# Performance work log

Hardware: AMD Instinct MI355X
Metric: run time of the kernel (lower is better)

Reference implementation:

```python
import jax, jax.numpy as jnp
import numpy as np


def _sepconv1x1(x, dw, pw, b):
    # SeparableConv2D with kernel=1: depthwise 1x1 = per-channel scale, then pointwise matmul
    return jnp.einsum('nhwc,cd->nhwd', x * dw, pw) + b


def setup_inputs() -> dict:
    key = jax.random.key(0)
    ks = jax.random.split(key, 12)
    N, H, W, C_in, C_red = 4, 64, 64, 256, 64
    s = 0.05  # small init so softmax logits are well-conditioned
    return {
        'feature_maps': jax.random.normal(ks[0], (N, H, W, C_in), jnp.float32),
        'global_channel_output': jax.random.normal(ks[1], (N, H, W, C_in), jnp.float32),
        'dw_q': jax.random.normal(ks[2], (C_in,), jnp.float32) * s,
        'pw_q': jax.random.normal(ks[3], (C_in, C_red), jnp.float32) * s,
        'b_q': jnp.zeros((C_red,), jnp.float32),
        'dw_k': jax.random.normal(ks[4], (C_in,), jnp.float32) * s,
        'pw_k': jax.random.normal(ks[5], (C_in, C_red), jnp.float32) * s,
        'b_k': jnp.zeros((C_red,), jnp.float32),
        'dw_v': jax.random.normal(ks[6], (C_in,), jnp.float32) * s,
        'pw_v': jax.random.normal(ks[7], (C_in, C_red), jnp.float32) * s,
        'b_v': jnp.zeros((C_red,), jnp.float32),
        'dw_a': jax.random.normal(ks[8], (C_red,), jnp.float32) * s,
        'pw_a': jax.random.normal(ks[9], (C_red, C_in), jnp.float32) * s,
        'b_a': jnp.zeros((C_in,), jnp.float32),
    }


def reference(feature_maps, global_channel_output,
              dw_q, pw_q, b_q, dw_k, pw_k, b_k, dw_v, pw_v, b_v,
              dw_a, pw_a, b_a):
    N, H, W, _ = feature_maps.shape
    q = _sepconv1x1(feature_maps, dw_q, pw_q, b_q)  # [N,H,W,Cr]
    k = _sepconv1x1(feature_maps, dw_k, pw_k, b_k)
    v = _sepconv1x1(feature_maps, dw_v, pw_v, b_v)
    Cr = q.shape[-1]
    q = q.reshape(N, H * W, Cr)
    k = k.reshape(N, H * W, Cr)
    v = v.reshape(N, H * W, Cr)
    # tf.matmul(key, query, transpose_b=True): scores[i,j] = key_i . query_j
    scores = jnp.einsum('nic,njc->nij', k, q)  # [N,HW,HW]
    scores = jax.nn.softmax(scores, axis=-1)
    # tf.matmul(value, scores, transpose_a=True) -> [N,Cr,HW]
    att = jnp.einsum('nic,nij->ncj', v, scores)
    # faithful raw reshape (as in the original TF code) from [N,Cr,HW] to [N,H,W,Cr]
    att = att.reshape(N, H, W, Cr)
    att = _sepconv1x1(att, dw_a, pw_a, b_a)  # [N,H,W,C_in]
    return global_channel_output * att + global_channel_output
```

## Files before the change

kernel.cpp:

```cpp
#include <hip/hip_runtime.h>
#include <hip/hip_bf16.h>

typedef __attribute__((ext_vector_type(8))) __bf16 bf16x8;
typedef __attribute__((ext_vector_type(2))) __bf16 bf16x2;
typedef __attribute__((ext_vector_type(4))) float floatx4;
typedef __attribute__((ext_vector_type(4))) unsigned short us4;
typedef __attribute__((ext_vector_type(8))) unsigned short us8;
typedef __attribute__((ext_vector_type(4))) short s16x4;
typedef __attribute__((ext_vector_type(2))) unsigned int uint2v;
typedef __attribute__((ext_vector_type(4))) unsigned int uint4v;

#define MFMA16(A, B, C) __builtin_amdgcn_mfma_f32_16x16x32_bf16((A), (B), (C), 0, 0, 0)
#define MFMA1K(A, B, C) __builtin_amdgcn_mfma_f32_16x16x16bf16_1k((A), (B), (C), 0, 0, 0)

#define LOG2E 1.44269504088896340736f

#if __has_builtin(__builtin_amdgcn_exp2f)
#define EXP2F(x) __builtin_amdgcn_exp2f(x)
#else
#define EXP2F(x) exp2f(x)
#endif

static __device__ __forceinline__ unsigned short f2bfbits(float f) {
    __hip_bfloat16 h = __float2bfloat16(f);
    union { __hip_bfloat16 h; unsigned short u; } cv;
    cv.h = h;
    return cv.u;
}
static __device__ __forceinline__ unsigned int rne32(float f) {
    unsigned int u = __builtin_bit_cast(unsigned int, f);
    return u + 0x7fffu + ((u >> 16) & 1u);
}
static __device__ __forceinline__ unsigned short rne16(float f) {
    return (unsigned short)(rne32(f) >> 16);
}

#if __has_builtin(__builtin_amdgcn_cvt_pk_bf16_f32)
static __device__ __forceinline__ s16x4 pack4(float e0, float e1, float e2, float e3) {
    bf16x2 lo = __builtin_amdgcn_cvt_pk_bf16_f32(e0, e1);
    bf16x2 hi = __builtin_amdgcn_cvt_pk_bf16_f32(e2, e3);
    uint2v u = {__builtin_bit_cast(unsigned int, lo), __builtin_bit_cast(unsigned int, hi)};
    return __builtin_bit_cast(s16x4, u);
}
static __device__ __forceinline__ bf16x8 cvt8(floatx4 a, floatx4 b) {
    bf16x2 p0 = __builtin_amdgcn_cvt_pk_bf16_f32(a[0], a[1]);
    bf16x2 p1 = __builtin_amdgcn_cvt_pk_bf16_f32(a[2], a[3]);
    bf16x2 p2 = __builtin_amdgcn_cvt_pk_bf16_f32(b[0], b[1]);
    bf16x2 p3 = __builtin_amdgcn_cvt_pk_bf16_f32(b[2], b[3]);
    uint4v u = {__builtin_bit_cast(unsigned int, p0), __builtin_bit_cast(unsigned int, p1),
                __builtin_bit_cast(unsigned int, p2), __builtin_bit_cast(unsigned int, p3)};
    return __builtin_bit_cast(bf16x8, u);
}
#else
static __device__ __forceinline__ s16x4 pack4(float e0, float e1, float e2, float e3) {
    unsigned int pa = __builtin_amdgcn_perm(rne32(e1), rne32(e0), 0x07060302u);
    unsigned int pb = __builtin_amdgcn_perm(rne32(e3), rne32(e2), 0x07060302u);
    uint2v u = {pa, pb};
    return __builtin_bit_cast(s16x4, u);
}
static __device__ __forceinline__ bf16x8 cvt8(floatx4 a, floatx4 b) {
    us8 u;
#pragma unroll
    for (int i = 0; i < 4; i++) { u[i] = rne16(a[i]); u[4 + i] = rne16(b[i]); }
    return __builtin_bit_cast(bf16x8, u);
}
#endif

static __device__ __forceinline__ bf16x8 load_bf8(const __hip_bfloat16* p) {
    return *reinterpret_cast<const bf16x8*>(p);
}
static __device__ __forceinline__ float bf2f(unsigned short u) {
    unsigned int w = ((unsigned int)u) << 16;
    return __builtin_bit_cast(float, w);
}


__global__ __launch_bounds__(256) void prep_w(
    const float* __restrict__ dwq, const float* __restrict__ pwq,
    const float* __restrict__ dwk, const float* __restrict__ pwk,
    const float* __restrict__ dwv, const float* __restrict__ pwv,
    __hip_bfloat16* __restrict__ wT)
{
    int idx = blockIdx.x * 256 + threadIdx.x;
    int p = idx >> 14;
    int r = idx & 16383;
    int d = r >> 8, c = r & 255;
    const float* dw = (p == 0) ? dwq : ((p == 1) ? dwk : dwv);
    const float* pw = (p == 0) ? pwq : ((p == 1) ? pwk : pwv);
    float scale = (p == 1) ? LOG2E : 1.0f;
    wT[idx] = __float2bfloat16(dw[c] * pw[c * 64 + d] * scale);
}

__global__ __launch_bounds__(256) void proj_qkv(
    const float* __restrict__ x,
    const __hip_bfloat16* __restrict__ wT,
    const float* __restrict__ bqp, const float* __restrict__ bkp,
    const float* __restrict__ bvp,
    __hip_bfloat16* __restrict__ qf, __hip_bfloat16* __restrict__ kf,
    __hip_bfloat16* __restrict__ vf)
{
    int wg = blockIdx.x * 4 + (threadIdx.x >> 6);
    int p = wg >> 10;
    int wid = wg & 1023;
    int lane = threadIdx.x & 63;
    int l15 = lane & 15, quad = lane >> 4;
    int strip = wid << 4;

    floatx4 acc[4];
#pragma unroll
    for (int t = 0; t < 4; t++) acc[t] = (floatx4){0.f, 0.f, 0.f, 0.f};

    const float* xrow = x + (strip + l15) * 256 + quad * 8;
    const __hip_bfloat16* wp = wT + p * 16384;
#pragma unroll
    for (int ks = 0; ks < 8; ks++) {
        floatx4 xa = *reinterpret_cast<const floatx4*>(xrow + ks * 32);
        floatx4 xb = *reinterpret_cast<const floatx4*>(xrow + ks * 32 + 4);
        bf16x8 a = cvt8(xa, xb);
#pragma unroll
        for (int t = 0; t < 4; t++) {
            bf16x8 b = load_bf8(wp + (t * 16 + l15) * 256 + ks * 32 + quad * 8);
            acc[t] = MFMA16(a, b, acc[t]);
        }
    }
    if (p < 2) {
        __hip_bfloat16* dst = (p == 0) ? qf : kf;
        const float* bias = (p == 0) ? bqp : bkp;
        float bscale = (p == 1) ? LOG2E : 1.0f;
#pragma unroll
        for (int t = 0; t < 4; t++) {
            float bsv = bias[t * 16 + l15] * bscale;
            int off0 = wid * 1024 + (t >> 1) * 512 +
                       (((((t & 1) << 1) | (l15 >> 3)) * 16 + quad * 4) * 8) + (l15 & 7);
#pragma unroll
            for (int r = 0; r < 4; r++)
                dst[off0 + r * 8] = __float2bfloat16(acc[t][r] + bsv);
        }
    } else {
#pragma unroll
        for (int t = 0; t < 4; t++) {
            float bsv = bvp[t * 16 + l15];
            us4 pk;
#pragma unroll
            for (int r = 0; r < 4; r++) pk[r] = f2bfbits(acc[t][r] + bsv);
            *reinterpret_cast<us4*>(vf + (wid * 4 + t) * 256 + lane * 4) = pk;
        }
    }
}

__global__ __launch_bounds__(512) void pass1_rl(
    const __hip_bfloat16* __restrict__ qf, const __hip_bfloat16* __restrict__ kf,
    const __hip_bfloat16* __restrict__ vf, __hip_bfloat16* __restrict__ vfs)
{
    int itg0 = blockIdx.x * 2;
    int n = itg0 >> 8;
    int jw = threadIdx.x >> 6;
    int lane = threadIdx.x & 63;
    int l15 = lane & 15, quad = lane >> 4;

    const __hip_bfloat16* kp = kf + itg0 * 1024 + lane * 8;
    bf16x8 a0 = load_bf8(kp);
    bf16x8 a1 = load_bf8(kp + 512);
    bf16x8 a2 = load_bf8(kp + 1024);
    bf16x8 a3 = load_bf8(kp + 1536);

    floatx4 lsA = (floatx4){0.f, 0.f, 0.f, 0.f};
    floatx4 lsB = (floatx4){0.f, 0.f, 0.f, 0.f};
    const __hip_bfloat16* qp0 = qf + (n * 256 + jw * 32) * 1024 + lane * 8;
    for (int it = 0; it < 16; it++, qp0 += 2048) {
        bf16x8 b0 = load_bf8(qp0);
        bf16x8 b1 = load_bf8(qp0 + 512);
        bf16x8 b2 = load_bf8(qp0 + 1024);
        bf16x8 b3 = load_bf8(qp0 + 1536);
        floatx4 z = (floatx4){0.f, 0.f, 0.f, 0.f};
        floatx4 sA0 = MFMA16(a1, b1, MFMA16(a0, b0, z));
        floatx4 sA1 = MFMA16(a1, b3, MFMA16(a0, b2, z));
        floatx4 sB0 = MFMA16(a3, b1, MFMA16(a2, b0, z));
        floatx4 sB1 = MFMA16(a3, b3, MFMA16(a2, b2, z));
#pragma unroll
        for (int r = 0; r < 4; r++) {
            lsA[r] += EXP2F(sA0[r]) + EXP2F(sA1[r]);
            lsB[r] += EXP2F(sB0[r]) + EXP2F(sB1[r]);
        }
    }
#pragma unroll
    for (int m = 1; m < 16; m <<= 1) {
#pragma unroll
        for (int r = 0; r < 4; r++) {
            lsA[r] += __shfl_xor(lsA[r], m, 64);
            lsB[r] += __shfl_xor(lsB[r], m, 64);
        }
    }
    __shared__ float red[8][32];
    __shared__ float rls[32];
    if (l15 == 0) {
#pragma unroll
        for (int r = 0; r < 4; r++) {
            red[jw][quad * 4 + r] = lsA[r];
            red[jw][16 + quad * 4 + r] = lsB[r];
        }
    }
    __syncthreads();
    if (threadIdx.x < 32) {
        float tot = 0.f;
#pragma unroll
        for (int w = 0; w < 8; w++) tot += red[w][threadIdx.x];
        rls[threadIdx.x] = 1.0f / tot;
    }
    __syncthreads();
    int m0 = threadIdx.x * 4;
    int toff = m0 >> 10;
    int mm = m0 & 1023;
    int t = mm >> 8;
    int l = (mm >> 2) & 63;
    int rb = toff * 16 + (l >> 4) * 4;
    us4 vv = *reinterpret_cast<const us4*>(
        reinterpret_cast<const unsigned short*>(vf) + itg0 * 1024 + m0);
    us4 ov;
#pragma unroll
    for (int r = 0; r < 4; r++) ov[r] = rne16(bf2f(vv[r]) * rls[rb + r]);
    *reinterpret_cast<us4*>(
        reinterpret_cast<unsigned short*>(vfs) + (itg0 + toff) * 1024 + l * 16 + t * 4) = ov;
}

template<int ITERS, int IHB>
__global__ __launch_bounds__(256) void pass2_att(
    const __hip_bfloat16* __restrict__ qf, const __hip_bfloat16* __restrict__ kf,
    const __hip_bfloat16* __restrict__ vfs,
    unsigned short* __restrict__ attp)
{
    int b = blockIdx.x;
    int ih = b & ((1 << IHB) - 1);
    int g = b >> IHB;
    int n = g >> 4;
    int jg = g & 15;
    int w = threadIdx.x >> 6;
    int jt0 = jg * 16 + w * 4;
    int lane = threadIdx.x & 63;
    int l15 = lane & 15, quad = lane >> 4;

    const __hip_bfloat16* qp = qf + (n * 256 + jt0) * 1024 + lane * 8;
    bf16x8 bq0a = load_bf8(qp);
    bf16x8 bq0b = load_bf8(qp + 512);
    bf16x8 bq1a = load_bf8(qp + 1024);
    bf16x8 bq1b = load_bf8(qp + 1536);
    bf16x8 bq2a = load_bf8(qp + 2048);
    bf16x8 bq2b = load_bf8(qp + 2560);
    bf16x8 bq3a = load_bf8(qp + 3072);
    bf16x8 bq3b = load_bf8(qp + 3584);

    floatx4 acc0[4], acc1[4], acc2[4], acc3[4];
#pragma unroll
    for (int t = 0; t < 4; t++) {
        acc0[t] = (floatx4){0.f, 0.f, 0.f, 0.f};
        acc1[t] = (floatx4){0.f, 0.f, 0.f, 0.f};
        acc2[t] = (floatx4){0.f, 0.f, 0.f, 0.f};
        acc3[t] = (floatx4){0.f, 0.f, 0.f, 0.f};
    }

    int it0 = n * 256 + ih * ITERS;
    const __hip_bfloat16* kp = kf + it0 * 1024 + lane * 8;
    const __hip_bfloat16* vp = vfs + it0 * 1024 + lane * 16;

    bf16x8 a0 = load_bf8(kp);
    bf16x8 a1 = load_bf8(kp + 512);
    us8 v01 = *reinterpret_cast<const us8*>(vp);
    us8 v23 = *reinterpret_cast<const us8*>(vp + 8);

    for (int it = 0; it < ITERS; it++) {
        bf16x8 na0, na1; us8 nv01, nv23;
        if (it + 1 < ITERS) {
            const __hip_bfloat16* kpn = kp + 1024;
            const __hip_bfloat16* vpn = vp + 1024;
            na0 = load_bf8(kpn);
            na1 = load_bf8(kpn + 512);
            nv01 = *reinterpret_cast<const us8*>(vpn);
            nv23 = *reinterpret_cast<const us8*>(vpn + 8);
        }
        floatx4 z = (floatx4){0.f, 0.f, 0.f, 0.f};
        floatx4 s0 = MFMA16(a1, bq0b, MFMA16(a0, bq0a, z));
        floatx4 s1 = MFMA16(a1, bq1b, MFMA16(a0, bq1a, z));
        floatx4 s2 = MFMA16(a1, bq2b, MFMA16(a0, bq2a, z));
        floatx4 s3 = MFMA16(a1, bq3b, MFMA16(a0, bq3a, z));
        s16x4 p0 = pack4(EXP2F(s0[0]), EXP2F(s0[1]), EXP2F(s0[2]), EXP2F(s0[3]));
        s16x4 p1 = pack4(EXP2F(s1[0]), EXP2F(s1[1]), EXP2F(s1[2]), EXP2F(s1[3]));
        s16x4 p2 = pack4(EXP2F(s2[0]), EXP2F(s2[1]), EXP2F(s2[2]), EXP2F(s2[3]));
        s16x4 p3 = pack4(EXP2F(s3[0]), EXP2F(s3[1]), EXP2F(s3[2]), EXP2F(s3[3]));
        s16x4 bv0 = __builtin_bit_cast(s16x4, __builtin_shufflevector(v01, v01, 0, 1, 2, 3));
        s16x4 bv1 = __builtin_bit_cast(s16x4, __builtin_shufflevector(v01, v01, 4, 5, 6, 7));
        s16x4 bv2 = __builtin_bit_cast(s16x4, __builtin_shufflevector(v23, v23, 0, 1, 2, 3));
        s16x4 bv3 = __builtin_bit_cast(s16x4, __builtin_shufflevector(v23, v23, 4, 5, 6, 7));
        acc0[0] = MFMA1K(p0, bv0, acc0[0]);
        acc1[0] = MFMA1K(p1, bv0, acc1[0]);
        acc2[0] = MFMA1K(p2, bv0, acc2[0]);
        acc3[0] = MFMA1K(p3, bv0, acc3[0]);
        acc0[1] = MFMA1K(p0, bv1, acc0[1]);
        acc1[1] = MFMA1K(p1, bv1, acc1[1]);
        acc2[1] = MFMA1K(p2, bv1, acc2[1]);
        acc3[1] = MFMA1K(p3, bv1, acc3[1]);
        acc0[2] = MFMA1K(p0, bv2, acc0[2]);
        acc1[2] = MFMA1K(p1, bv2, acc1[2]);
        acc2[2] = MFMA1K(p2, bv2, acc2[2]);
        acc3[2] = MFMA1K(p3, bv2, acc3[2]);
        acc0[3] = MFMA1K(p0, bv3, acc0[3]);
        acc1[3] = MFMA1K(p1, bv3, acc1[3]);
        acc2[3] = MFMA1K(p2, bv3, acc2[3]);
        acc3[3] = MFMA1K(p3, bv3, acc3[3]);
        a0 = na0; a1 = na1; v01 = nv01; v23 = nv23;
        kp += 1024; vp += 1024;
    }
    unsigned short* op0 = attp + ih * 1048576;
#pragma unroll
    for (int t = 0; t < 4; t++) {
        s16x4 k0 = pack4(acc0[t][0], acc0[t][1], acc0[t][2], acc0[t][3]);
        s16x4 k1 = pack4(acc1[t][0], acc1[t][1], acc1[t][2], acc1[t][3]);
        s16x4 k2 = pack4(acc2[t][0], acc2[t][1], acc2[t][2], acc2[t][3]);
        s16x4 k3 = pack4(acc3[t][0], acc3[t][1], acc3[t][2], acc3[t][3]);
        unsigned short* op = op0 + (n * 64 + t * 16 + l15) * 4096 + jt0 * 16 + quad * 4;
        *reinterpret_cast<s16x4*>(op) = k0;
        *reinterpret_cast<s16x4*>(op + 16) = k1;
        *reinterpret_cast<s16x4*>(op + 32) = k2;
        *reinterpret_cast<s16x4*>(op + 48) = k3;
    }
}

template<int NPART>
__global__ __launch_bounds__(256) void final_out(
    const unsigned short* __restrict__ attp, const float* __restrict__ gco,
    const float* __restrict__ dwa, const float* __restrict__ pwa,
    const float* __restrict__ ba, float* __restrict__ out)
{
    int b = blockIdx.x;
    int n = b >> 9;
    int hh = (b >> 3) & 63;
    int w0 = (b & 7) << 3;
    __shared__ float g[512];
    int tid = threadIdx.x;
    const unsigned short* ap = attp + (n * 64 + hh) * 4096 + w0 * 64;
    {
        int jj0 = tid * 2;
        float v0 = 0.f, v1 = 0.f;
#pragma unroll
        for (int ph = 0; ph < NPART; ph++) {
            unsigned int u = *reinterpret_cast<const unsigned int*>(ap + ph * 1048576 + jj0);
            v0 += bf2f((unsigned short)(u & 0xffffu));
            v1 += bf2f((unsigned short)(u >> 16));
        }
        g[jj0] = v0 * dwa[jj0 & 63];
        g[jj0 + 1] = v1 * dwa[(jj0 + 1) & 63];
    }
    __syncthreads();
    float acc[8];
#pragma unroll
    for (int w = 0; w < 8; w++) acc[w] = 0.f;
    for (int cc = 0; cc < 64; cc++) {
        float p = pwa[cc * 256 + tid];
#pragma unroll
        for (int w = 0; w < 8; w++) acc[w] += g[w * 64 + cc] * p;
    }
    float bb = ba[tid];
#pragma unroll
    for (int w = 0; w < 8; w++) {
        int pos = (n * 64 + hh) * 64 + w0 + w;
        float gv = gco[pos * 256 + tid];
        out[pos * 256 + tid] = gv * (acc[w] + bb) + gv;
    }
}

extern "C" void kernel_launch(void* const* d_in, const int* in_sizes, int n_in,
                              void* d_out, int out_size, void* d_ws, size_t ws_size,
                              hipStream_t stream) {
    const float* x   = (const float*)d_in[0];
    const float* gco = (const float*)d_in[1];
    const float* dwq = (const float*)d_in[2];
    const float* pwq = (const float*)d_in[3];
    const float* bq  = (const float*)d_in[4];
    const float* dwk = (const float*)d_in[5];
    const float* pwk = (const float*)d_in[6];
    const float* bk  = (const float*)d_in[7];
    const float* dwv = (const float*)d_in[8];
    const float* pwv = (const float*)d_in[9];
    const float* bv  = (const float*)d_in[10];
    const float* dwa = (const float*)d_in[11];
    const float* pwa = (const float*)d_in[12];
    const float* ba  = (const float*)d_in[13];
    float* out = (float*)d_out;

    char* ws = (char*)d_ws;
    __hip_bfloat16* wT  = (__hip_bfloat16*)ws;
    __hip_bfloat16* qf  = (__hip_bfloat16*)(ws + 98304);
    __hip_bfloat16* kf  = (__hip_bfloat16*)(ws + 2195456);
    __hip_bfloat16* vf  = (__hip_bfloat16*)(ws + 4292608);
    __hip_bfloat16* vfs = (__hip_bfloat16*)(ws + 6389760);
    unsigned short* attp = (unsigned short*)(ws + 8486912);

    prep_w<<<192, 256, 0, stream>>>(dwq, pwq, dwk, pwk, dwv, pwv, wT);
    proj_qkv<<<768, 256, 0, stream>>>(x, wT, bq, bk, bv, qf, kf, vf);
    pass1_rl<<<512, 512, 0, stream>>>(qf, kf, vf, vfs);
    pass2_att<32, 3><<<512, 256, 0, stream>>>(qf, kf, vfs, attp);
    final_out<8><<<2048, 256, 0, stream>>>(attp, gco, dwa, pwa, ba, out);
}
```

Baseline: 177.4 us.

## Fuse weight prep into projection, deepen load prefetch, remap pass2 blocks per XCD

Removes the separate prep_w launch by having each projection block build its swizzled bf16 weight tile in shared memory. Both attention passes now unroll by two with double-depth register prefetch of Q/K/V fragments, so more loads are in flight while MFMA and exp work runs. Pass2 block indices are remapped so blocks that share key/value ranges land on the same XCD, aiming for better L2 reuse. The cost is redundant weight construction in every projection block and higher register pressure in the attention loops.

After: 169.7 us. -4.3%, faster.

```diff
diff --git a/kernel.cpp b/kernel.cpp
--- a/kernel.cpp
+++ b/kernel.cpp
@@ -75,43 +75,46 @@
 }
 
 
-__global__ __launch_bounds__(256) void prep_w(
+__global__ __launch_bounds__(256) void proj_qkv(
+    const float* __restrict__ x,
     const float* __restrict__ dwq, const float* __restrict__ pwq,
     const float* __restrict__ dwk, const float* __restrict__ pwk,
     const float* __restrict__ dwv, const float* __restrict__ pwv,
-    __hip_bfloat16* __restrict__ wT)
-{
-    int idx = blockIdx.x * 256 + threadIdx.x;
-    int p = idx >> 14;
-    int r = idx & 16383;
-    int d = r >> 8, c = r & 255;
-    const float* dw = (p == 0) ? dwq : ((p == 1) ? dwk : dwv);
-    const float* pw = (p == 0) ? pwq : ((p == 1) ? pwk : pwv);
-    float scale = (p == 1) ? LOG2E : 1.0f;
-    wT[idx] = __float2bfloat16(dw[c] * pw[c * 64 + d] * scale);
-}
-
-__global__ __launch_bounds__(256) void proj_qkv(
-    const float* __restrict__ x,
-    const __hip_bfloat16* __restrict__ wT,
     const float* __restrict__ bqp, const float* __restrict__ bkp,
     const float* __restrict__ bvp,
     __hip_bfloat16* __restrict__ qf, __hip_bfloat16* __restrict__ kf,
     __hip_bfloat16* __restrict__ vf)
 {
-    int wg = blockIdx.x * 4 + (threadIdx.x >> 6);
-    int p = wg >> 10;
-    int wid = wg & 1023;
-    int lane = threadIdx.x & 63;
+    __shared__ __hip_bfloat16 wle[16384];
+    int b = blockIdx.x;
+    int p = b >> 8;
+    int tg = b & 255;
+    int tid = threadIdx.x;
+
+    const float* dw = (p == 0) ? dwq : ((p == 1) ? dwk : dwv);
+    const float* pw = (p == 0) ? pwq : ((p == 1) ? pwk : pwv);
+    float scale = (p == 1) ? LOG2E : 1.0f;
+
+    {
+        float dwc = dw[tid];
+#pragma unroll
+        for (int k = 0; k < 64; k++) {
+            int idx = (k * 256 + tid) ^ ((k & 7) << 3);
+            wle[idx] = __float2bfloat16(dwc * pw[tid * 64 + k] * scale);
+        }
+    }
+    __syncthreads();
+
+    int wv = tid >> 6;
+    int wid = tg * 4 + wv;
+    int lane = tid & 63;
     int l15 = lane & 15, quad = lane >> 4;
-    int strip = wid << 4;
 
     floatx4 acc[4];
 #pragma unroll
     for (int t = 0; t < 4; t++) acc[t] = (floatx4){0.f, 0.f, 0.f, 0.f};
 
-    const float* xrow = x + (strip + l15) * 256 + quad * 8;
-    const __hip_bfloat16* wp = wT + p * 16384;
+    const float* xrow = x + (wid * 16 + l15) * 256 + quad * 8;
 #pragma unroll
     for (int ks = 0; ks < 8; ks++) {
         floatx4 xa = *reinterpret_cast<const floatx4*>(xrow + ks * 32);
@@ -119,8 +122,9 @@
         bf16x8 a = cvt8(xa, xb);
 #pragma unroll
         for (int t = 0; t < 4; t++) {
-            bf16x8 b = load_bf8(wp + (t * 16 + l15) * 256 + ks * 32 + quad * 8);
-            acc[t] = MFMA16(a, b, acc[t]);
+            int j0 = ((t * 16 + l15) * 256 + ks * 32 + quad * 8) ^ ((l15 & 7) << 3);
+            bf16x8 bfr = *reinterpret_cast<const bf16x8*>(&wle[j0]);
+            acc[t] = MFMA16(a, bfr, acc[t]);
         }
     }
     if (p < 2) {
@@ -147,6 +151,19 @@
         }
     }
 }
+
+#define P1STEP(B0, B1, B2, B3) do {                                        \
+    floatx4 z = (floatx4){0.f, 0.f, 0.f, 0.f};                             \
+    floatx4 sA0 = MFMA16(a1, (B1), MFMA16(a0, (B0), z));                   \
+    floatx4 sA1 = MFMA16(a1, (B3), MFMA16(a0, (B2), z));                   \
+    floatx4 sB0 = MFMA16(a3, (B1), MFMA16(a2, (B0), z));                   \
+    floatx4 sB1 = MFMA16(a3, (B3), MFMA16(a2, (B2), z));                   \
+    _Pragma("unroll")                                                      \
+    for (int r = 0; r < 4; r++) {                                          \
+        lsA[r] += EXP2F(sA0[r]) + EXP2F(sA1[r]);                           \
+        lsB[r] += EXP2F(sB0[r]) + EXP2F(sB1[r]);                           \
+    }                                                                      \
+} while (0)
 
 __global__ __launch_bounds__(512) void pass1_rl(
     const __hip_bfloat16* __restrict__ qf, const __hip_bfloat16* __restrict__ kf,
@@ -167,21 +184,30 @@
     floatx4 lsA = (floatx4){0.f, 0.f, 0.f, 0.f};
     floatx4 lsB = (floatx4){0.f, 0.f, 0.f, 0.f};
     const __hip_bfloat16* qp0 = qf + (n * 256 + jw * 32) * 1024 + lane * 8;
-    for (int it = 0; it < 16; it++, qp0 += 2048) {
-        bf16x8 b0 = load_bf8(qp0);
-        bf16x8 b1 = load_bf8(qp0 + 512);
-        bf16x8 b2 = load_bf8(qp0 + 1024);
-        bf16x8 b3 = load_bf8(qp0 + 1536);
-        floatx4 z = (floatx4){0.f, 0.f, 0.f, 0.f};
-        floatx4 sA0 = MFMA16(a1, b1, MFMA16(a0, b0, z));
-        floatx4 sA1 = MFMA16(a1, b3, MFMA16(a0, b2, z));
-        floatx4 sB0 = MFMA16(a3, b1, MFMA16(a2, b0, z));
-        floatx4 sB1 = MFMA16(a3, b3, MFMA16(a2, b2, z));
-#pragma unroll
-        for (int r = 0; r < 4; r++) {
-            lsA[r] += EXP2F(sA0[r]) + EXP2F(sA1[r]);
-            lsB[r] += EXP2F(sB0[r]) + EXP2F(sB1[r]);
-        }
+
+    bf16x8 s0b0 = load_bf8(qp0);
+    bf16x8 s0b1 = load_bf8(qp0 + 512);
+    bf16x8 s0b2 = load_bf8(qp0 + 1024);
+    bf16x8 s0b3 = load_bf8(qp0 + 1536);
+    bf16x8 s1b0 = load_bf8(qp0 + 2048);
+    bf16x8 s1b1 = load_bf8(qp0 + 2560);
+    bf16x8 s1b2 = load_bf8(qp0 + 3072);
+    bf16x8 s1b3 = load_bf8(qp0 + 3584);
+
+    for (int it = 0; it < 16; it += 2) {
+        bf16x8 n0 = load_bf8(qp0 + 4096);
+        bf16x8 n1 = load_bf8(qp0 + 4608);
+        bf16x8 n2 = load_bf8(qp0 + 5120);
+        bf16x8 n3 = load_bf8(qp0 + 5632);
+        P1STEP(s0b0, s0b1, s0b2, s0b3);
+        s0b0 = n0; s0b1 = n1; s0b2 = n2; s0b3 = n3;
+        bf16x8 m0 = load_bf8(qp0 + 6144);
+        bf16x8 m1 = load_bf8(qp0 + 6656);
+        bf16x8 m2 = load_bf8(qp0 + 7168);
+        bf16x8 m3 = load_bf8(qp0 + 7680);
+        P1STEP(s1b0, s1b1, s1b2, s1b3);
+        s1b0 = m0; s1b1 = m1; s1b2 = m2; s1b3 = m3;
+        qp0 += 4096;
     }
 #pragma unroll
     for (int m = 1; m < 16; m <<= 1) {
@@ -223,17 +249,48 @@
         reinterpret_cast<unsigned short*>(vfs) + (itg0 + toff) * 1024 + l * 16 + t * 4) = ov;
 }
 
-template<int ITERS, int IHB>
+#define P2STEP(KA, KB, VA, VB) do {                                            \
+    floatx4 z = (floatx4){0.f, 0.f, 0.f, 0.f};                                 \
+    floatx4 s0 = MFMA16((KB), bq0b, MFMA16((KA), bq0a, z));                    \
+    floatx4 s1 = MFMA16((KB), bq1b, MFMA16((KA), bq1a, z));                    \
+    floatx4 s2 = MFMA16((KB), bq2b, MFMA16((KA), bq2a, z));                    \
+    floatx4 s3 = MFMA16((KB), bq3b, MFMA16((KA), bq3a, z));                    \
+    s16x4 p0 = pack4(EXP2F(s0[0]), EXP2F(s0[1]), EXP2F(s0[2]), EXP2F(s0[3])); \
+    s16x4 p1 = pack4(EXP2F(s1[0]), EXP2F(s1[1]), EXP2F(s1[2]), EXP2F(s1[3])); \
+    s16x4 p2 = pack4(EXP2F(s2[0]), EXP2F(s2[1]), EXP2F(s2[2]), EXP2F(s2[3])); \
+    s16x4 p3 = pack4(EXP2F(s3[0]), EXP2F(s3[1]), EXP2F(s3[2]), EXP2F(s3[3])); \
+    s16x4 bv0 = __builtin_bit_cast(s16x4, __builtin_shufflevector((VA), (VA), 0, 1, 2, 3)); \
+    s16x4 bv1 = __builtin_bit_cast(s16x4, __builtin_shufflevector((VA), (VA), 4, 5, 6, 7)); \
+    s16x4 bv2 = __builtin_bit_cast(s16x4, __builtin_shufflevector((VB), (VB), 0, 1, 2, 3)); \
+    s16x4 bv3 = __builtin_bit_cast(s16x4, __builtin_shufflevector((VB), (VB), 4, 5, 6, 7)); \
+    acc0[0] = MFMA1K(p0, bv0, acc0[0]);                                        \
+    acc1[0] = MFMA1K(p1, bv0, acc1[0]);                                        \
+    acc2[0] = MFMA1K(p2, bv0, acc2[0]);                                        \
+    acc3[0] = MFMA1K(p3, bv0, acc3[0]);                                        \
+    acc0[1] = MFMA1K(p0, bv1, acc0[1]);                                        \
+    acc1[1] = MFMA1K(p1, bv1, acc1[1]);                                        \
+    acc2[1] = MFMA1K(p2, bv1, acc2[1]);                                        \
+    acc3[1] = MFMA1K(p3, bv1, acc3[1]);                                        \
+    acc0[2] = MFMA1K(p0, bv2, acc0[2]);                                        \
+    acc1[2] = MFMA1K(p1, bv2, acc1[2]);                                        \
+    acc2[2] = MFMA1K(p2, bv2, acc2[2]);                                        \
+    acc3[2] = MFMA1K(p3, bv2, acc3[2]);                                        \
+    acc0[3] = MFMA1K(p0, bv3, acc0[3]);                                        \
+    acc1[3] = MFMA1K(p1, bv3, acc1[3]);                                        \
+    acc2[3] = MFMA1K(p2, bv3, acc2[3]);                                        \
+    acc3[3] = MFMA1K(p3, bv3, acc3[3]);                                        \
+} while (0)
+
 __global__ __launch_bounds__(256) void pass2_att(
     const __hip_bfloat16* __restrict__ qf, const __hip_bfloat16* __restrict__ kf,
     const __hip_bfloat16* __restrict__ vfs,
     unsigned short* __restrict__ attp)
 {
     int b = blockIdx.x;
-    int ih = b & ((1 << IHB) - 1);
-    int g = b >> IHB;
-    int n = g >> 4;
-    int jg = g & 15;
+    int xcd = b & 7, slot = b >> 3;
+    int g = xcd + 8 * (slot >> 4);
+    int jg = slot & 15;
+    int n = g >> 3, ih = g & 7;
     int w = threadIdx.x >> 6;
     int jt0 = jg * 16 + w * 4;
     int lane = threadIdx.x & 63;
@@ -258,56 +315,33 @@
         acc3[t] = (floatx4){0.f, 0.f, 0.f, 0.f};
     }
 
-    int it0 = n * 256 + ih * ITERS;
+    int it0 = n * 256 + ih * 32;
     const __hip_bfloat16* kp = kf + it0 * 1024 + lane * 8;
     const __hip_bfloat16* vp = vfs + it0 * 1024 + lane * 16;
 
-    bf16x8 a0 = load_bf8(kp);
-    bf16x8 a1 = load_bf8(kp + 512);
-    us8 v01 = *reinterpret_cast<const us8*>(vp);
-    us8 v23 = *reinterpret_cast<const us8*>(vp + 8);
-
-    for (int it = 0; it < ITERS; it++) {
-        bf16x8 na0, na1; us8 nv01, nv23;
-        if (it + 1 < ITERS) {
-            const __hip_bfloat16* kpn = kp + 1024;
-            const __hip_bfloat16* vpn = vp + 1024;
-            na0 = load_bf8(kpn);
-            na1 = load_bf8(kpn + 512);
-            nv01 = *reinterpret_cast<const us8*>(vpn);
-            nv23 = *reinterpret_cast<const us8*>(vpn + 8);
-        }
-        floatx4 z = (floatx4){0.f, 0.f, 0.f, 0.f};
-        floatx4 s0 = MFMA16(a1, bq0b, MFMA16(a0, bq0a, z));
-        floatx4 s1 = MFMA16(a1, bq1b, MFMA16(a0, bq1a, z));
-        floatx4 s2 = MFMA16(a1, bq2b, MFMA16(a0, bq2a, z));
-        floatx4 s3 = MFMA16(a1, bq3b, MFMA16(a0, bq3a, z));
-        s16x4 p0 = pack4(EXP2F(s0[0]), EXP2F(s0[1]), EXP2F(s0[2]), EXP2F(s0[3]));
-        s16x4 p1 = pack4(EXP2F(s1[0]), EXP2F(s1[1]), EXP2F(s1[2]), EXP2F(s1[3]));
-        s16x4 p2 = pack4(EXP2F(s2[0]), EXP2F(s2[1]), EXP2F(s2[2]), EXP2F(s2[3]));
-        s16x4 p3 = pack4(EXP2F(s3[0]), EXP2F(s3[1]), EXP2F(s3[2]), EXP2F(s3[3]));
-        s16x4 bv0 = __builtin_bit_cast(s16x4, __builtin_shufflevector(v01, v01, 0, 1, 2, 3));
-        s16x4 bv1 = __builtin_bit_cast(s16x4, __builtin_shufflevector(v01, v01, 4, 5, 6, 7));
-        s16x4 bv2 = __builtin_bit_cast(s16x4, __builtin_shufflevector(v23, v23, 0, 1, 2, 3));
-        s16x4 bv3 = __builtin_bit_cast(s16x4, __builtin_shufflevector(v23, v23, 4, 5, 6, 7));
-        acc0[0] = MFMA1K(p0, bv0, acc0[0]);
-        acc1[0] = MFMA1K(p1, bv0, acc1[0]);
-        acc2[0] = MFMA1K(p2, bv0, acc2[0]);
-        acc3[0] = MFMA1K(p3, bv0, acc3[0]);
-        acc0[1] = MFMA1K(p0, bv1, acc0[1]);
-        acc1[1] = MFMA1K(p1, bv1, acc1[1]);
-        acc2[1] = MFMA1K(p2, bv1, acc2[1]);
-        acc3[1] = MFMA1K(p3, bv1, acc3[1]);
-        acc0[2] = MFMA1K(p0, bv2, acc0[2]);
-        acc1[2] = MFMA1K(p1, bv2, acc1[2]);
-        acc2[2] = MFMA1K(p2, bv2, acc2[2]);
-        acc3[2] = MFMA1K(p3, bv2, acc3[2]);
-        acc0[3] = MFMA1K(p0, bv3, acc0[3]);
-        acc1[3] = MFMA1K(p1, bv3, acc1[3]);
-        acc2[3] = MFMA1K(p2, bv3, acc2[3]);
-        acc3[3] = MFMA1K(p3, bv3, acc3[3]);
-        a0 = na0; a1 = na1; v01 = nv01; v23 = nv23;
-        kp += 1024; vp += 1024;
+    bf16x8 kA0 = load_bf8(kp);
+    bf16x8 kB0 = load_bf8(kp + 512);
+    us8 vA0 = *reinterpret_cast<const us8*>(vp);
+    us8 vB0 = *reinterpret_cast<const us8*>(vp + 8);
+    bf16x8 kA1 = load_bf8(kp + 1024);
+    bf16x8 kB1 = load_bf8(kp + 1536);
+    us8 vA1 = *reinterpret_cast<const us8*>(vp + 1024);
+    us8 vB1 = *reinterpret_cast<const us8*>(vp + 1024 + 8);
+
+    for (int it = 0; it < 32; it += 2) {
+        bf16x8 nkA = load_bf8(kp + 2048);
+        bf16x8 nkB = load_bf8(kp + 2560);
+        us8 nvA = *reinterpret_cast<const us8*>(vp + 2048);
+        us8 nvB = *reinterpret_cast<const us8*>(vp + 2048 + 8);
+        P2STEP(kA0, kB0, vA0, vB0);
+        kA0 = nkA; kB0 = nkB; vA0 = nvA; vB0 = nvB;
+        bf16x8 mkA = load_bf8(kp + 3072);
+        bf16x8 mkB = load_bf8(kp + 3584);
+        us8 mvA = *reinterpret_cast<const us8*>(vp + 3072);
+        us8 mvB = *reinterpret_cast<const us8*>(vp + 3072 + 8);
+        P2STEP(kA1, kB1, vA1, vB1);
+        kA1 = mkA; kB1 = mkB; vA1 = mvA; vB1 = mvB;
+        kp += 2048; vp += 2048;
     }
     unsigned short* op0 = attp + ih * 1048576;
 #pragma unroll
@@ -387,16 +421,15 @@
     float* out = (float*)d_out;
 
     char* ws = (char*)d_ws;
-    __hip_bfloat16* wT  = (__hip_bfloat16*)ws;
     __hip_bfloat16* qf  = (__hip_bfloat16*)(ws + 98304);
     __hip_bfloat16* kf  = (__hip_bfloat16*)(ws + 2195456);
     __hip_bfloat16* vf  = (__hip_bfloat16*)(ws + 4292608);
     __hip_bfloat16* vfs = (__hip_bfloat16*)(ws + 6389760);
     unsigned short* attp = (unsigned short*)(ws + 8486912);
 
-    prep_w<<<192, 256, 0, stream>>>(dwq, pwq, dwk, pwk, dwv, pwv, wT);
-    proj_qkv<<<768, 256, 0, stream>>>(x, wT, bq, bk, bv, qf, kf, vf);
+    proj_qkv<<<768, 256, 0, stream>>>(x, dwq, pwq, dwk, pwk, dwv, pwv,
+                                      bq, bk, bv, qf, kf, vf);
     pass1_rl<<<512, 512, 0, stream>>>(qf, kf, vf, vfs);
-    pass2_att<32, 3><<<512, 256, 0, stream>>>(qf, kf, vfs, attp);
+    pass2_att<<<512, 256, 0, stream>>>(qf, kf, vfs, attp);
     final_out<8><<<2048, 256, 0, stream>>>(attp, gco, dwa, pwa, ba, out);
 }
```
